# Optimization experiments

Measured on AMD Instinct MI355X. Metric: run time of the kernel, lower is better.

Reference implementation:

```python
import jax, jax.numpy as jnp
import numpy as np

N, C, H, W = 8, 256, 31, 31
HIDDEN, OUT = 512, 256


def setup_inputs() -> dict:
    key = jax.random.key(0)
    k0, k1, k2, k3, k4 = jax.random.split(key, 5)
    x = jax.random.normal(k0, (N, C, H, W), dtype=jnp.float32)
    # Linear params (torch nn.Linear layout: [out_features, in_features])
    W1 = jax.random.normal(k1, (HIDDEN, C), dtype=jnp.float32) * (1.0 / np.sqrt(C))
    b1 = jax.random.normal(k2, (HIDDEN,), dtype=jnp.float32) * 0.01
    W2 = jax.random.normal(k3, (OUT, HIDDEN), dtype=jnp.float32) * (1.0 / np.sqrt(HIDDEN))
    b2 = jax.random.normal(k4, (OUT,), dtype=jnp.float32) * 0.01
    return {"x": x, "W1": W1, "b1": b1, "W2": W2, "b2": b2}


def _normalized_adjacency(n, h, w):
    M = n * h * w
    idx = jnp.arange(M)
    blk = idx // (h * w)          # sample id of each node
    pos = idx % (h * w)           # spatial position within sample
    # block-diagonal all-ones per sample
    same_block = (blk[:, None] == blk[None, :]).astype(jnp.float32)
    # identity link between consecutive samples (disjoint from block-diag)
    neighbor = ((jnp.abs(blk[:, None] - blk[None, :]) == 1)
                & (pos[:, None] == pos[None, :])).astype(jnp.float32)
    A = same_block + neighbor + jnp.eye(M, dtype=jnp.float32)
    deg = A.sum(axis=1)
    dinv = jnp.where(deg > 0, deg ** -0.5, 0.0)
    return A * dinv[:, None] * dinv[None, :]  # D^-1/2 A D^-1/2


def reference(x, W1, b1, W2, b2):
    n, c, h, w = x.shape
    weight = _normalized_adjacency(n, h, w)                 # [M, M]
    nodes = x.transpose(0, 2, 3, 1).reshape(-1, c)          # [M, C]
    hid = jax.nn.leaky_relu(weight @ nodes @ W1.T + b1)     # [M, HIDDEN]
    hid = jax.nn.leaky_relu(weight @ hid @ W2.T + b2)       # [M, OUT]
    hid = hid.reshape(n, h, w, -1).transpose(0, 3, 1, 2)    # [N, OUT, H, W]
    return hid.max(axis=0, keepdims=True)                   # [1, OUT, H, W]
```

## Files before the change

kernel.cpp:

```cpp
#include <hip/hip_runtime.h>
#include <math.h>

#define NS   8
#define CC   256
#define PP   961
#define MM   7688
#define MP   7744
#define HID  512
#define OUTC 256

typedef _Float16 h16;
using half8   = __attribute__((ext_vector_type(8))) _Float16;
using floatx4 = __attribute__((ext_vector_type(4))) float;

#define AS1 __attribute__((address_space(1)))
#define AS3 __attribute__((address_space(3)))

__device__ __forceinline__ float dinv_of(int b) {
    return (b == 0 || b == NS - 1) ? 0.0322245515f : 0.0322078318f;
}

__global__ void prep(const float* __restrict__ W1, const float* __restrict__ W2,
                     h16* __restrict__ w1h, h16* __restrict__ w2h,
                     const float* __restrict__ x, float* __restrict__ S1,
                     float* __restrict__ SY) {
    int blk = blockIdx.x, tid = threadIdx.x;
    if (blk < 256) {
        bool second = blk >= 128;
        const float* src = second ? W2 : W1;
        h16* dst = second ? w2h : w1h;
        int i = ((blk & 127) * 256 + tid) * 4;
        float4 v = *(const float4*)(src + i);
        dst[i + 0] = (h16)v.x; dst[i + 1] = (h16)v.y;
        dst[i + 2] = (h16)v.z; dst[i + 3] = (h16)v.w;
    } else if (blk < 2304) {
        int bc = blk - 256;
        const float* src = x + (size_t)bc * PP;
        float s = 0.f;
        for (int i = tid; i < PP; i += 256) s += src[i];
        __shared__ float red[256];
        red[tid] = s;
        __syncthreads();
        for (int off = 128; off > 0; off >>= 1) {
            if (tid < off) red[tid] += red[tid + off];
            __syncthreads();
        }
        if (tid == 0) S1[bc] = red[0];
    } else {
        int i = (blk - 2304) * 256 + tid;
        SY[i] = 0.f;
    }
}

__global__ void build_g1(const float* __restrict__ x, const float* __restrict__ S1,
                         h16* __restrict__ G1) {
    int pt = blockIdx.x, ct = blockIdx.y, b = blockIdx.z;
    int p0 = pt * 32, c0 = ct * 32;
    float db  = dinv_of(b);
    float wm  = (b > 0)      ? db * dinv_of(b - 1) : 0.f;
    float wp  = (b < NS - 1) ? db * dinv_of(b + 1) : 0.f;
    float db2 = db * db;
    __shared__ float t[32][33];
    int j = threadIdx.x & 31, i0 = threadIdx.x >> 5;
    int p = p0 + j;
    bool pv = (p < PP);
    #pragma unroll
    for (int r = 0; r < 4; ++r) {
        int i = i0 + r * 8;
        int c = c0 + i;
        float v = 0.f;
        if (pv) {
            size_t base = ((size_t)b * CC + c) * PP + p;
            float xb = x[base];
            float xm = (b > 0)      ? x[base - (size_t)CC * PP] : 0.f;
            float xp = (b < NS - 1) ? x[base + (size_t)CC * PP] : 0.f;
            v = db2 * (S1[b * CC + c] + xb) + wm * xm + wp * xp;
        }
        t[i][j] = v;
    }
    __syncthreads();
    int ii = threadIdx.x & 31, jj0 = threadIdx.x >> 5;
    #pragma unroll
    for (int r = 0; r < 4; ++r) {
        int jj = jj0 + r * 8;
        int pw = p0 + jj;
        if (pw < PP)
            G1[((size_t)b * PP + pw) * CC + c0 + ii] = (h16)t[ii][jj];
    }
}

template<int KD, bool ACT, bool DO_SUM, typename OutT>
__global__ __launch_bounds__(256) void mfma_gemm(
    const h16* __restrict__ A,
    const h16* __restrict__ B,
    const float* __restrict__ bias,
    OutT* __restrict__ C,
    float* __restrict__ SY,
    int M, int Nc)
{
    __shared__ __align__(16) h16 As[64 * 64];
    __shared__ __align__(16) h16 Bs[64 * 64];
    int tid = threadIdx.x, wave = tid >> 6, lane = tid & 63;
    int m0 = blockIdx.x * 64, n0 = blockIdx.y * 64;
    int sro = lane >> 3;
    int sch = (lane & 7) ^ sro;
    const h16* ga0 = A + (size_t)(m0 + wave * 16 + sro) * KD + sch * 8;
    const h16* gb0 = B + (size_t)(n0 + wave * 16 + sro) * KD + sch * 8;
    h16* la0 = &As[(wave * 16) * 64];
    h16* la1 = &As[(wave * 16 + 8) * 64];
    h16* lb0 = &Bs[(wave * 16) * 64];
    h16* lb1 = &Bs[(wave * 16 + 8) * 64];
    int fr = lane & 15, fq = lane >> 4;
    floatx4 acc[4] = {{0.f,0.f,0.f,0.f},{0.f,0.f,0.f,0.f},{0.f,0.f,0.f,0.f},{0.f,0.f,0.f,0.f}};
    for (int kk = 0; kk < KD; kk += 64) {
        __builtin_amdgcn_global_load_lds((const AS1 void*)(const void*)(ga0 + kk),
                                         (AS3 void*)(void*)la0, 16, 0, 0);
        __builtin_amdgcn_global_load_lds((const AS1 void*)(const void*)(ga0 + 8 * KD + kk),
                                         (AS3 void*)(void*)la1, 16, 0, 0);
        __builtin_amdgcn_global_load_lds((const AS1 void*)(const void*)(gb0 + kk),
                                         (AS3 void*)(void*)lb0, 16, 0, 0);
        __builtin_amdgcn_global_load_lds((const AS1 void*)(const void*)(gb0 + 8 * KD + kk),
                                         (AS3 void*)(void*)lb1, 16, 0, 0);
        __syncthreads();
        #pragma unroll
        for (int ks = 0; ks < 2; ++ks) {
            int slot = (ks * 4 + fq) ^ (fr & 7);
            half8 bf = *(const half8*)&Bs[(wave * 16 + fr) * 64 + slot * 8];
            #pragma unroll
            for (int mb = 0; mb < 4; ++mb) {
                half8 af = *(const half8*)&As[(mb * 16 + fr) * 64 + slot * 8];
                acc[mb] = __builtin_amdgcn_mfma_f32_16x16x32_f16(af, bf, acc[mb], 0, 0, 0);
            }
        }
        __syncthreads();
    }
    int col = n0 + wave * 16 + fr;
    float bv = ACT ? bias[col] : 0.f;
    float s_lo = 0.f, s_hi = 0.f;
    int blo = m0 / 961;
    int mcut = (blo + 1) * 961;
    #pragma unroll
    for (int mb = 0; mb < 4; ++mb) {
        #pragma unroll
        for (int r = 0; r < 4; ++r) {
            int m = m0 + mb * 16 + fq * 4 + r;
            if (m < M) {
                float v = acc[mb][r] + bv;
                if (ACT) v = (v >= 0.f) ? v : 0.01f * v;
                C[(size_t)m * Nc + col] = (OutT)v;
                if (DO_SUM) { if (m < mcut) s_lo += v; else s_hi += v; }
            }
        }
    }
    if (DO_SUM) {
        s_lo += __shfl_xor(s_lo, 16);
        s_lo += __shfl_xor(s_lo, 32);
        s_hi += __shfl_xor(s_hi, 16);
        s_hi += __shfl_xor(s_hi, 32);
        if (fq == 0) {
            atomicAdd(&SY[blo * Nc + col], s_lo);
            int bhi = (m0 + 63) / 961;
            if (bhi != blo && bhi < NS) atomicAdd(&SY[bhi * Nc + col], s_hi);
        }
    }
}

__global__ void final_max(const float* __restrict__ Y, const float* __restrict__ SY,
                          const float* __restrict__ b2, float* __restrict__ out) {
    int pt = blockIdx.x, ot = blockIdx.y;
    int p0 = pt * 32, o0 = ot * 32;
    __shared__ float t[32][33];
    int i = threadIdx.x & 31, j0 = threadIdx.x >> 5;
    int o = o0 + i;
    float bias = b2[o];
    #pragma unroll
    for (int r = 0; r < 4; ++r) {
        int j = j0 + r * 8;
        int p = p0 + j;
        float vmax = -INFINITY;
        if (p < PP) {
            float y[NS];
            #pragma unroll
            for (int b = 0; b < NS; ++b)
                y[b] = Y[((size_t)b * PP + p) * OUTC + o];
            #pragma unroll
            for (int b = 0; b < NS; ++b) {
                float db = dinv_of(b);
                float a = db * (SY[b * OUTC + o] + y[b]);
                if (b > 0)      a += dinv_of(b - 1) * y[b - 1];
                if (b < NS - 1) a += dinv_of(b + 1) * y[b + 1];
                float z = db * a + bias;
                z = (z >= 0.f) ? z : 0.01f * z;
                vmax = fmaxf(vmax, z);
            }
        }
        t[j][i] = vmax;
    }
    __syncthreads();
    int jj = threadIdx.x & 31, ii0 = threadIdx.x >> 5;
    #pragma unroll
    for (int r = 0; r < 4; ++r) {
        int ii = ii0 + r * 8;
        int pw = p0 + jj;
        if (pw < PP)
            out[(size_t)(o0 + ii) * PP + pw] = t[jj][ii];
    }
}

extern "C" void kernel_launch(void* const* d_in, const int* in_sizes, int n_in,
                              void* d_out, int out_size, void* d_ws, size_t ws_size,
                              hipStream_t stream) {
    const float* x  = (const float*)d_in[0];
    const float* W1 = (const float*)d_in[1];
    const float* b1 = (const float*)d_in[2];
    const float* W2 = (const float*)d_in[3];
    const float* b2 = (const float*)d_in[4];
    float* out = (float*)d_out;
    float* ws  = (float*)d_ws;

    float* S1  = ws;
    float* SY  = ws + 2048;
    h16*  w1h  = (h16*)(ws + 4096);
    h16*  w2h  = (h16*)(ws + 69632);
    h16*  G1   = (h16*)(ws + 135168);
    h16*  H1   = (h16*)(ws + 1126400);
    float* Y   = ws + 3108864;

    prep<<<2312, 256, 0, stream>>>(W1, W2, w1h, w2h, x, S1, SY);
    build_g1<<<dim3(31, 8, NS), 256, 0, stream>>>(x, S1, G1);
    mfma_gemm<CC, true, false, h16><<<dim3(MP / 64, HID / 64), 256, 0, stream>>>(
        G1, w1h, b1, H1, nullptr, MM, HID);
    mfma_gemm<HID, false, true, float><<<dim3(MP / 64, OUTC / 64), 256, 0, stream>>>(
        H1, w2h, nullptr, Y, SY, MM, OUTC);
    final_max<<<dim3(31, 8), 256, 0, stream>>>(Y, SY, b2, out);
}
```

Measured before the change: 95.70 us.

## Fold prep kernel into build_g1 and GEMMs, convert weights in-kernel

Removes the separate prep kernel. Per-channel sums of x are now computed inside each build_g1 block, and SY zeroing moves into build_g1. Each GEMM block now loads its whole fp32 weight slice, converts it to fp16 and stages it in shared memory up front, instead of streaming pre-converted fp16 weights each k-step. This drops one launch and one pass over the data, but adds redundant x reads for the sums (every pt block re-reads its channels). It also adds larger LDS use in GEMM2 (64KB for B), which may lower occupancy.

```diff
diff --git a/kernel.cpp b/kernel.cpp
--- a/kernel.cpp
+++ b/kernel.cpp
@@ -20,42 +20,26 @@
     return (b == 0 || b == NS - 1) ? 0.0322245515f : 0.0322078318f;
 }
 
-__global__ void prep(const float* __restrict__ W1, const float* __restrict__ W2,
-                     h16* __restrict__ w1h, h16* __restrict__ w2h,
-                     const float* __restrict__ x, float* __restrict__ S1,
-                     float* __restrict__ SY) {
-    int blk = blockIdx.x, tid = threadIdx.x;
-    if (blk < 256) {
-        bool second = blk >= 128;
-        const float* src = second ? W2 : W1;
-        h16* dst = second ? w2h : w1h;
-        int i = ((blk & 127) * 256 + tid) * 4;
-        float4 v = *(const float4*)(src + i);
-        dst[i + 0] = (h16)v.x; dst[i + 1] = (h16)v.y;
-        dst[i + 2] = (h16)v.z; dst[i + 3] = (h16)v.w;
-    } else if (blk < 2304) {
-        int bc = blk - 256;
-        const float* src = x + (size_t)bc * PP;
-        float s = 0.f;
-        for (int i = tid; i < PP; i += 256) s += src[i];
-        __shared__ float red[256];
-        red[tid] = s;
-        __syncthreads();
-        for (int off = 128; off > 0; off >>= 1) {
-            if (tid < off) red[tid] += red[tid + off];
-            __syncthreads();
-        }
-        if (tid == 0) S1[bc] = red[0];
-    } else {
-        int i = (blk - 2304) * 256 + tid;
-        SY[i] = 0.f;
-    }
-}
-
-__global__ void build_g1(const float* __restrict__ x, const float* __restrict__ S1,
-                         h16* __restrict__ G1) {
+__global__ void build_g1(const float* __restrict__ x, h16* __restrict__ G1,
+                         float* __restrict__ SY) {
     int pt = blockIdx.x, ct = blockIdx.y, b = blockIdx.z;
     int p0 = pt * 32, c0 = ct * 32;
+    if (pt == 0 && ct == 0) SY[b * OUTC + threadIdx.x] = 0.f;
+
+    __shared__ float sS1[32];
+    int wave = threadIdx.x >> 6, lane = threadIdx.x & 63;
+    #pragma unroll
+    for (int rr = 0; rr < 8; ++rr) {
+        int i = wave * 8 + rr;
+        const float* src = x + ((size_t)b * CC + c0 + i) * PP;
+        float s = 0.f;
+        for (int k = lane; k < PP; k += 64) s += src[k];
+        #pragma unroll
+        for (int off = 32; off; off >>= 1) s += __shfl_xor(s, off);
+        if (lane == 0) sS1[i] = s;
+    }
+    __syncthreads();
+
     float db  = dinv_of(b);
     float wm  = (b > 0)      ? db * dinv_of(b - 1) : 0.f;
     float wp  = (b < NS - 1) ? db * dinv_of(b + 1) : 0.f;
@@ -74,7 +58,7 @@
             float xb = x[base];
             float xm = (b > 0)      ? x[base - (size_t)CC * PP] : 0.f;
             float xp = (b < NS - 1) ? x[base + (size_t)CC * PP] : 0.f;
-            v = db2 * (S1[b * CC + c] + xb) + wm * xm + wp * xp;
+            v = db2 * (sS1[i] + xb) + wm * xm + wp * xp;
         }
         t[i][j] = v;
     }
@@ -92,40 +76,52 @@
 template<int KD, bool ACT, bool DO_SUM, typename OutT>
 __global__ __launch_bounds__(256) void mfma_gemm(
     const h16* __restrict__ A,
-    const h16* __restrict__ B,
+    const float* __restrict__ Bf,
     const float* __restrict__ bias,
     OutT* __restrict__ C,
     float* __restrict__ SY,
     int M, int Nc)
 {
+    constexpr int NT = KD / 64;
     __shared__ __align__(16) h16 As[64 * 64];
-    __shared__ __align__(16) h16 Bs[64 * 64];
+    __shared__ __align__(16) h16 Bs[NT][64 * 64];
     int tid = threadIdx.x, wave = tid >> 6, lane = tid & 63;
     int m0 = blockIdx.x * 64, n0 = blockIdx.y * 64;
+
+    #pragma unroll
+    for (int t = 0; t < NT; ++t) {
+        #pragma unroll
+        for (int it = 0; it < 2; ++it) {
+            int task = it * 256 + tid;
+            int r = task >> 3, c = task & 7;
+            const float* src = Bf + (size_t)(n0 + r) * KD + t * 64 + c * 8;
+            float4 v0 = *(const float4*)(src);
+            float4 v1 = *(const float4*)(src + 4);
+            half8 h = { (h16)v0.x, (h16)v0.y, (h16)v0.z, (h16)v0.w,
+                        (h16)v1.x, (h16)v1.y, (h16)v1.z, (h16)v1.w };
+            *(half8*)&Bs[t][r * 64 + ((c ^ (r & 7)) * 8)] = h;
+        }
+    }
+
     int sro = lane >> 3;
     int sch = (lane & 7) ^ sro;
     const h16* ga0 = A + (size_t)(m0 + wave * 16 + sro) * KD + sch * 8;
-    const h16* gb0 = B + (size_t)(n0 + wave * 16 + sro) * KD + sch * 8;
     h16* la0 = &As[(wave * 16) * 64];
     h16* la1 = &As[(wave * 16 + 8) * 64];
-    h16* lb0 = &Bs[(wave * 16) * 64];
-    h16* lb1 = &Bs[(wave * 16 + 8) * 64];
     int fr = lane & 15, fq = lane >> 4;
     floatx4 acc[4] = {{0.f,0.f,0.f,0.f},{0.f,0.f,0.f,0.f},{0.f,0.f,0.f,0.f},{0.f,0.f,0.f,0.f}};
-    for (int kk = 0; kk < KD; kk += 64) {
-        __builtin_amdgcn_global_load_lds((const AS1 void*)(const void*)(ga0 + kk),
+
+    #pragma unroll
+    for (int t = 0; t < NT; ++t) {
+        __builtin_amdgcn_global_load_lds((const AS1 void*)(const void*)(ga0 + t * 64),
                                          (AS3 void*)(void*)la0, 16, 0, 0);
-        __builtin_amdgcn_global_load_lds((const AS1 void*)(const void*)(ga0 + 8 * KD + kk),
+        __builtin_amdgcn_global_load_lds((const AS1 void*)(const void*)(ga0 + 8 * KD + t * 64),
                                          (AS3 void*)(void*)la1, 16, 0, 0);
-        __builtin_amdgcn_global_load_lds((const AS1 void*)(const void*)(gb0 + kk),
-                                         (AS3 void*)(void*)lb0, 16, 0, 0);
-        __builtin_amdgcn_global_load_lds((const AS1 void*)(const void*)(gb0 + 8 * KD + kk),
-                                         (AS3 void*)(void*)lb1, 16, 0, 0);
         __syncthreads();
         #pragma unroll
         for (int ks = 0; ks < 2; ++ks) {
             int slot = (ks * 4 + fq) ^ (fr & 7);
-            half8 bf = *(const half8*)&Bs[(wave * 16 + fr) * 64 + slot * 8];
+            half8 bf = *(const half8*)&Bs[t][(wave * 16 + fr) * 64 + slot * 8];
             #pragma unroll
             for (int mb = 0; mb < 4; ++mb) {
                 half8 af = *(const half8*)&As[(mb * 16 + fr) * 64 + slot * 8];
@@ -218,19 +214,15 @@
     float* out = (float*)d_out;
     float* ws  = (float*)d_ws;
 
-    float* S1  = ws;
-    float* SY  = ws + 2048;
-    h16*  w1h  = (h16*)(ws + 4096);
-    h16*  w2h  = (h16*)(ws + 69632);
-    h16*  G1   = (h16*)(ws + 135168);
-    h16*  H1   = (h16*)(ws + 1126400);
-    float* Y   = ws + 3108864;
-
-    prep<<<2312, 256, 0, stream>>>(W1, W2, w1h, w2h, x, S1, SY);
-    build_g1<<<dim3(31, 8, NS), 256, 0, stream>>>(x, S1, G1);
+    float* SY  = ws;
+    h16*  G1   = (h16*)(ws + 2048);
+    h16*  H1   = (h16*)(ws + 993280);
+    float* Y   = ws + 2975744;
+
+    build_g1<<<dim3(31, 8, NS), 256, 0, stream>>>(x, G1, SY);
     mfma_gemm<CC, true, false, h16><<<dim3(MP / 64, HID / 64), 256, 0, stream>>>(
-        G1, w1h, b1, H1, nullptr, MM, HID);
+        G1, W1, b1, H1, nullptr, MM, HID);
     mfma_gemm<HID, false, true, float><<<dim3(MP / 64, OUTC / 64), 256, 0, stream>>>(
-        H1, w2h, nullptr, Y, SY, MM, OUTC);
+        H1, W2, nullptr, Y, SY, MM, OUTC);
     final_max<<<dim3(31, 8), 256, 0, stream>>>(Y, SY, b2, out);
 }
```

Result: slower. 133.6 us (+39.6%).

## Fuse G1 build into prep kernel and fold per-sample sum term into GEMM epilogue

Applied to the files above, without the earlier changes.

Removes the dependency of G1 construction on the per-sample channel sums by moving the db^2*S1 term out of G1. The term is instead computed in the first GEMM epilogue as a per-column dot product of W1 and S1. This lets the x-transpose, the weight conversion and the sum reduction run in one launch, dropping a kernel launch and its serialization. In exchange, each GEMM block now redoes a small fp32 dot product with global reads of W1 and S1. The sum reduction also switches to wave shuffles and the weight conversion to vectorized half4 stores.

```diff
diff --git a/kernel.cpp b/kernel.cpp
--- a/kernel.cpp
+++ b/kernel.cpp
@@ -10,6 +10,7 @@
 #define OUTC 256
 
 typedef _Float16 h16;
+using half4   = __attribute__((ext_vector_type(4))) _Float16;
 using half8   = __attribute__((ext_vector_type(8))) _Float16;
 using floatx4 = __attribute__((ext_vector_type(4))) float;
 
@@ -20,80 +21,78 @@
     return (b == 0 || b == NS - 1) ? 0.0322245515f : 0.0322078318f;
 }
 
-__global__ void prep(const float* __restrict__ W1, const float* __restrict__ W2,
-                     h16* __restrict__ w1h, h16* __restrict__ w2h,
-                     const float* __restrict__ x, float* __restrict__ S1,
-                     float* __restrict__ SY) {
+__global__ void fused_prep(const float* __restrict__ x,
+                           const float* __restrict__ W1, const float* __restrict__ W2,
+                           h16* __restrict__ w1h, h16* __restrict__ w2h,
+                           float* __restrict__ S1, h16* __restrict__ G1,
+                           float* __restrict__ SY) {
     int blk = blockIdx.x, tid = threadIdx.x;
-    if (blk < 256) {
-        bool second = blk >= 128;
+    if (blk < 1984) {
+        int pt = blk % 31, rem = blk / 31;
+        int ct = rem & 7, b = rem >> 3;
+        int p0 = pt * 32, c0 = ct * 32;
+        float db  = dinv_of(b);
+        float wm  = (b > 0)      ? db * dinv_of(b - 1) : 0.f;
+        float wp  = (b < NS - 1) ? db * dinv_of(b + 1) : 0.f;
+        float db2 = db * db;
+        __shared__ float t[32][33];
+        int j = tid & 31, i0 = tid >> 5;
+        int p = p0 + j;
+        bool pv = (p < PP);
+        #pragma unroll
+        for (int r = 0; r < 4; ++r) {
+            int i = i0 + r * 8;
+            int c = c0 + i;
+            float v = 0.f;
+            if (pv) {
+                size_t base = ((size_t)b * CC + c) * PP + p;
+                float xb = x[base];
+                float xm = (b > 0)      ? x[base - (size_t)CC * PP] : 0.f;
+                float xp = (b < NS - 1) ? x[base + (size_t)CC * PP] : 0.f;
+                v = db2 * xb + wm * xm + wp * xp;
+            }
+            t[i][j] = v;
+        }
+        __syncthreads();
+        int ii = tid & 31, jj0 = tid >> 5;
+        #pragma unroll
+        for (int r = 0; r < 4; ++r) {
+            int jj = jj0 + r * 8;
+            int pw = p0 + jj;
+            if (pw < PP)
+                G1[((size_t)b * PP + pw) * CC + c0 + ii] = (h16)t[ii][jj];
+        }
+    } else if (blk < 2240) {
+        int k = blk - 1984;
+        bool second = k >= 128;
         const float* src = second ? W2 : W1;
         h16* dst = second ? w2h : w1h;
-        int i = ((blk & 127) * 256 + tid) * 4;
+        int i = ((k & 127) * 256 + tid) * 4;
         float4 v = *(const float4*)(src + i);
-        dst[i + 0] = (h16)v.x; dst[i + 1] = (h16)v.y;
-        dst[i + 2] = (h16)v.z; dst[i + 3] = (h16)v.w;
-    } else if (blk < 2304) {
-        int bc = blk - 256;
-        const float* src = x + (size_t)bc * PP;
+        half4 h = { (h16)v.x, (h16)v.y, (h16)v.z, (h16)v.w };
+        *(half4*)(dst + i) = h;
+    } else if (blk < 2752) {
+        int wave = tid >> 6, lane = tid & 63;
+        int row = (blk - 2240) * 4 + wave;
+        const float* src = x + (size_t)row * PP;
         float s = 0.f;
-        for (int i = tid; i < PP; i += 256) s += src[i];
-        __shared__ float red[256];
-        red[tid] = s;
-        __syncthreads();
-        for (int off = 128; off > 0; off >>= 1) {
-            if (tid < off) red[tid] += red[tid + off];
-            __syncthreads();
-        }
-        if (tid == 0) S1[bc] = red[0];
+        for (int i = lane; i < PP; i += 64) s += src[i];
+        #pragma unroll
+        for (int off = 32; off; off >>= 1) s += __shfl_xor(s, off);
+        if (lane == 0) S1[row] = s;
     } else {
-        int i = (blk - 2304) * 256 + tid;
+        int i = (blk - 2752) * 256 + tid;
         SY[i] = 0.f;
     }
 }
 
-__global__ void build_g1(const float* __restrict__ x, const float* __restrict__ S1,
-                         h16* __restrict__ G1) {
-    int pt = blockIdx.x, ct = blockIdx.y, b = blockIdx.z;
-    int p0 = pt * 32, c0 = ct * 32;
-    float db  = dinv_of(b);
-    float wm  = (b > 0)      ? db * dinv_of(b - 1) : 0.f;
-    float wp  = (b < NS - 1) ? db * dinv_of(b + 1) : 0.f;
-    float db2 = db * db;
-    __shared__ float t[32][33];
-    int j = threadIdx.x & 31, i0 = threadIdx.x >> 5;
-    int p = p0 + j;
-    bool pv = (p < PP);
-    #pragma unroll
-    for (int r = 0; r < 4; ++r) {
-        int i = i0 + r * 8;
-        int c = c0 + i;
-        float v = 0.f;
-        if (pv) {
-            size_t base = ((size_t)b * CC + c) * PP + p;
-            float xb = x[base];
-            float xm = (b > 0)      ? x[base - (size_t)CC * PP] : 0.f;
-            float xp = (b < NS - 1) ? x[base + (size_t)CC * PP] : 0.f;
-            v = db2 * (S1[b * CC + c] + xb) + wm * xm + wp * xp;
-        }
-        t[i][j] = v;
-    }
-    __syncthreads();
-    int ii = threadIdx.x & 31, jj0 = threadIdx.x >> 5;
-    #pragma unroll
-    for (int r = 0; r < 4; ++r) {
-        int jj = jj0 + r * 8;
-        int pw = p0 + jj;
-        if (pw < PP)
-            G1[((size_t)b * PP + pw) * CC + c0 + ii] = (h16)t[ii][jj];
-    }
-}
-
-template<int KD, bool ACT, bool DO_SUM, typename OutT>
+template<int KD, bool ACT, bool DO_T1, bool DO_SUM, typename OutT>
 __global__ __launch_bounds__(256) void mfma_gemm(
     const h16* __restrict__ A,
     const h16* __restrict__ B,
     const float* __restrict__ bias,
+    const float* __restrict__ W1f,
+    const float* __restrict__ S1,
     OutT* __restrict__ C,
     float* __restrict__ SY,
     int M, int Nc)
@@ -136,19 +135,41 @@
     }
     int col = n0 + wave * 16 + fr;
     float bv = ACT ? bias[col] : 0.f;
-    float s_lo = 0.f, s_hi = 0.f;
     int blo = m0 / 961;
     int mcut = (blo + 1) * 961;
+    float t_lo = 0.f, t_hi = 0.f;
+    if (DO_T1) {
+        int bhiT = (m0 + 63) / 961;
+        if (bhiT >= NS) bhiT = blo;
+        const float4* wrow = (const float4*)(W1f + (size_t)col * KD + fq * 64);
+        const float4* slo  = (const float4*)(S1 + (size_t)blo  * KD + fq * 64);
+        const float4* shi  = (const float4*)(S1 + (size_t)bhiT * KD + fq * 64);
+        #pragma unroll
+        for (int i = 0; i < 16; ++i) {
+            float4 w = wrow[i];
+            float4 a = slo[i];
+            float4 b = shi[i];
+            t_lo += w.x * a.x + w.y * a.y + w.z * a.z + w.w * a.w;
+            t_hi += w.x * b.x + w.y * b.y + w.z * b.z + w.w * b.w;
+        }
+        t_lo += __shfl_xor(t_lo, 16); t_lo += __shfl_xor(t_lo, 32);
+        t_hi += __shfl_xor(t_hi, 16); t_hi += __shfl_xor(t_hi, 32);
+        float dlo = dinv_of(blo);  t_lo *= dlo * dlo;
+        float dhi = dinv_of(bhiT); t_hi *= dhi * dhi;
+    }
+    float s_lo = 0.f, s_hi = 0.f;
     #pragma unroll
     for (int mb = 0; mb < 4; ++mb) {
         #pragma unroll
         for (int r = 0; r < 4; ++r) {
             int m = m0 + mb * 16 + fq * 4 + r;
             if (m < M) {
+                bool lo = (m < mcut);
                 float v = acc[mb][r] + bv;
+                if (DO_T1) v += lo ? t_lo : t_hi;
                 if (ACT) v = (v >= 0.f) ? v : 0.01f * v;
                 C[(size_t)m * Nc + col] = (OutT)v;
-                if (DO_SUM) { if (m < mcut) s_lo += v; else s_hi += v; }
+                if (DO_SUM) { if (lo) s_lo += v; else s_hi += v; }
             }
         }
     }
@@ -226,11 +247,10 @@
     h16*  H1   = (h16*)(ws + 1126400);
     float* Y   = ws + 3108864;
 
-    prep<<<2312, 256, 0, stream>>>(W1, W2, w1h, w2h, x, S1, SY);
-    build_g1<<<dim3(31, 8, NS), 256, 0, stream>>>(x, S1, G1);
-    mfma_gemm<CC, true, false, h16><<<dim3(MP / 64, HID / 64), 256, 0, stream>>>(
-        G1, w1h, b1, H1, nullptr, MM, HID);
-    mfma_gemm<HID, false, true, float><<<dim3(MP / 64, OUTC / 64), 256, 0, stream>>>(
-        H1, w2h, nullptr, Y, SY, MM, OUTC);
+    fused_prep<<<2760, 256, 0, stream>>>(x, W1, W2, w1h, w2h, S1, G1, SY);
+    mfma_gemm<CC, true, true, false, h16><<<dim3(MP / 64, HID / 64), 256, 0, stream>>>(
+        G1, w1h, b1, W1, S1, H1, nullptr, MM, HID);
+    mfma_gemm<HID, false, false, true, float><<<dim3(MP / 64, OUTC / 64), 256, 0, stream>>>(
+        H1, w2h, nullptr, nullptr, nullptr, Y, SY, MM, OUTC);
     final_max<<<dim3(31, 8), 256, 0, stream>>>(Y, SY, b2, out);
 }
```

Result: slower. 107.3 us (+12.1%).
